# Performance work log

Measured on AMD Instinct MI355X. Metric: run time of the kernel, lower is better.

## Reference

```python
import jax, jax.numpy as jnp
import numpy as np

N_NEURONS, RANK, N_CONV, LY, LX, BATCH = 8192, 1, 64, 36, 36, 256


def setup_inputs() -> dict:
    key = jax.random.key(0)
    k1, k2, k3, k4 = jax.random.split(key, 4)
    conv = jax.random.normal(k1, (BATCH, N_CONV, LY, LX), dtype=jnp.float32)
    Wc = 0.01 * jax.random.normal(k2, (N_NEURONS, RANK, N_CONV), dtype=jnp.float32)
    Wy = 0.01 * jax.random.normal(k3, (N_NEURONS, RANK, LY), dtype=jnp.float32)
    Wx = 0.01 * jax.random.normal(k4, (N_NEURONS, RANK, LX), dtype=jnp.float32)
    bias = jnp.zeros((N_NEURONS,), dtype=jnp.float32)
    return {"conv": conv, "Wc": Wc, "Wy": Wy, "Wx": Wx, "bias": bias}


def reference(conv, Wc, Wy, Wx, bias):
    # yx_separable, rank == 1 path of Readout.forward:
    #   pred = einsum('nrc,nry,icyx,nrx->in', Wc, Wy, conv, Wx)
    #   pred = elu(pred + bias)
    # Staged contraction: build per-neuron rank-1 spatial filter, contract
    # spatial dims first (small y*x=1296), then channels.
    Wyx = jnp.einsum('nry,nrx->nryx', Wy, Wx)              # [N, R, Ly, Lx]
    s = jnp.einsum('icyx,nryx->inrc', conv, Wyx)           # [B, N, R, C]
    pred = jnp.einsum('inrc,nrc->in', s, Wc)               # [B, N]
    return jax.nn.elu(pred + bias)
```

## Files before the change

### kernel.cpp

```cpp
#include <hip/hip_runtime.h>
#include <hip/hip_bf16.h>

#define NNEUR 8192
#define NCONV 64
#define LYC   36
#define LXC   36
#define BATCH 256
#define KRAW  1296
#define KPAD  1344
#define KITER 21
#define MROWS 16384
#define BM 256
#define BN 128
#define BK 64
#define ACH_PER_IT 2048
#define BCH_PER_IT 1024
#define A_TILE_H   (KITER * ACH_PER_IT * 8)
#define B_TILE_H   (KITER * BCH_PER_IT * 8)

typedef __attribute__((ext_vector_type(8))) _Float16 half8;
typedef __attribute__((ext_vector_type(4))) float f32x4;
typedef __attribute__((ext_vector_type(16))) float f32x16;

__device__ __forceinline__ void async_copy16(const void* g, void* l) {
  __builtin_amdgcn_global_load_lds(
      (const __attribute__((address_space(1))) void*)g,
      (__attribute__((address_space(3))) void*)l, 16, 0, 0);
}

__global__ __launch_bounds__(256) void prep_kernel(
    const float* __restrict__ conv, const float* __restrict__ Wy,
    const float* __restrict__ Wx, _Float16* __restrict__ A,
    _Float16* __restrict__ B) {
  const int t = threadIdx.x;
  const int bx = blockIdx.x;
  const int tile = blockIdx.y;
  const int slot = t & 7;
  half8 h;
  if (bx < 168) {
    const int it = bx >> 3, i = bx & 7;
    const int r = (t >> 3) + 32 * i;
    const int c = (slot - r) & 7;
    const int k0 = it * 64 + c * 8;
    const int grow = tile * BM + r;
    if (k0 < KRAW) {
      const float* s = conv + (size_t)grow * KRAW + k0;
#pragma unroll
      for (int e = 0; e < 8; e++) h[e] = (_Float16)s[e];
    } else {
#pragma unroll
      for (int e = 0; e < 8; e++) h[e] = (_Float16)0.f;
    }
    *(half8*)(A + (size_t)tile * A_TILE_H + ((size_t)bx * 256 + t) * 8) = h;
  } else {
    const int bx4 = bx - 168;
    const int it = bx4 >> 2, i = bx4 & 3;
    const int r = (t >> 3) + 32 * i;
    const int c = (slot - r) & 7;
    const int k0 = it * 64 + c * 8;
    const int n = tile * BN + r;
#pragma unroll
    for (int e = 0; e < 8; e++) {
      const int k = k0 + e;
      float v = 0.f;
      if (k < KRAW) {
        const int y = k / LXC;
        const int x = k - y * LXC;
        v = Wy[n * LYC + y] * Wx[n * LXC + x] * 256.f;
      }
      h[e] = (_Float16)v;
    }
    *(half8*)(B + (size_t)tile * B_TILE_H + ((size_t)bx4 * 256 + t) * 8) = h;
  }
}

__global__ __launch_bounds__(256, 3) void gemm_fused_kernel(
    const _Float16* __restrict__ A, const _Float16* __restrict__ B,
    const float* __restrict__ Wc, const float* __restrict__ bias,
    float* __restrict__ out) {
  __shared__ _Float16 As[BM * BK];
  __shared__ _Float16 Bs[BN * BK];

  const int bid = blockIdx.x;
  const int l = bid >> 3;
  const int ntile = (bid & 7) * 8 + (l & 7);
  const int mtile = l >> 3;
  const int tileN = ntile * BN;
  const int tileM = mtile * BM;

  const int t = threadIdx.x;
  const int lane = t & 63;
  const int wave = t >> 6;
  const int wm = wave >> 1, wn = wave & 1;
  const int r32 = lane & 31, hh = lane >> 5;

  f32x16 acc[4][2] = {};

  const _Float16* pA = A + (size_t)mtile * A_TILE_H;
  const _Float16* pB = B + (size_t)ntile * B_TILE_H;
  _Float16* lA = As + t * 8;
  _Float16* lB = Bs + t * 8;

  for (int it = 0; it < KITER; it++) {
    const _Float16* sA = pA + (size_t)it * (ACH_PER_IT * 8) + t * 8;
    const _Float16* sB = pB + (size_t)it * (BCH_PER_IT * 8) + t * 8;
#pragma unroll
    for (int i = 0; i < 8; i++) async_copy16(sA + i * 2048, lA + i * 2048);
#pragma unroll
    for (int i = 0; i < 4; i++) async_copy16(sB + i * 2048, lB + i * 2048);
    __syncthreads();

#pragma unroll
    for (int ks = 0; ks < 4; ks++) {
      const int cc = 2 * ks + hh;
      half8 bf[2];
#pragma unroll
      for (int nb = 0; nb < 2; nb++) {
        const int r = wn * 64 + nb * 32 + r32;
        bf[nb] = *(const half8*)(Bs + r * 64 + ((cc + r) & 7) * 8);
      }
#pragma unroll
      for (int mb = 0; mb < 4; mb++) {
        const int r = wm * 128 + mb * 32 + r32;
        const half8 af = *(const half8*)(As + r * 64 + ((cc + r) & 7) * 8);
#pragma unroll
        for (int nb = 0; nb < 2; nb++)
          acc[mb][nb] = __builtin_amdgcn_mfma_f32_32x32x16_f16(
              af, bf[nb], acc[mb][nb], 0, 0, 0);
      }
    }
    __syncthreads();
  }

  const int ibase = mtile * 4 + wm * 2;
  float v[2][2];
#pragma unroll
  for (int nb = 0; nb < 2; nb++) {
    const int n_g = tileN + wn * 64 + nb * 32 + r32;
    const float* wc = Wc + (size_t)n_g * NCONV;
    f32x4 w[2][4];
#pragma unroll
    for (int hf = 0; hf < 2; hf++)
#pragma unroll
      for (int g = 0; g < 4; g++)
        w[hf][g] = *(const f32x4*)(wc + hf * 32 + hh * 4 + g * 8);
#pragma unroll
    for (int img = 0; img < 2; img++) {
      float p = 0.f;
#pragma unroll
      for (int hf = 0; hf < 2; hf++)
#pragma unroll
        for (int g = 0; g < 4; g++)
#pragma unroll
          for (int q = 0; q < 4; q++)
            p += acc[img * 2 + hf][nb][g * 4 + q] * w[hf][g][q];
      p += __shfl_xor(p, 32);
      v[img][nb] = p;
    }
  }
  const int img = ibase + hh;
#pragma unroll
  for (int nb = 0; nb < 2; nb++) {
    const int n_out = tileN + wn * 64 + nb * 32 + r32;
    float z = v[hh][nb] * 0.00390625f + bias[n_out];
    z = z > 0.f ? z : (__expf(z) - 1.f);
    out[(size_t)img * NNEUR + n_out] = z;
  }
}

extern "C" void kernel_launch(void* const* d_in, const int* in_sizes, int n_in,
                              void* d_out, int out_size, void* d_ws,
                              size_t ws_size, hipStream_t stream) {
  const float* conv = (const float*)d_in[0];
  const float* Wc = (const float*)d_in[1];
  const float* Wy = (const float*)d_in[2];
  const float* Wx = (const float*)d_in[3];
  const float* bias = (const float*)d_in[4];
  float* out = (float*)d_out;

  _Float16* Abuf = (_Float16*)d_ws;
  _Float16* Bbuf = (_Float16*)((char*)d_ws + (size_t)MROWS * KPAD * 2);

  prep_kernel<<<dim3(252, 64), 256, 0, stream>>>(conv, Wy, Wx, Abuf, Bbuf);
  gemm_fused_kernel<<<4096, 256, 0, stream>>>(Abuf, Bbuf, Wc, bias, out);
}
```

Measured before the change: 482.4 us.

## Double-buffer LDS tiles and enlarge GEMM block to 256x256 with 8 waves

Changes the GEMM tile from 256x128 to 256x256 with 512 threads (8 waves, 2x4 layout), which halves the grid and reuses each A tile across twice as many neurons. It adds double-buffered LDS so the async global-to-LDS copies for the next K step overlap with MFMA work on the current one, using manual vmcnt waits and barriers. It also raises wave priority around the MFMA loop. The prep kernel's B layout is reorganised to match the 256-wide N tiles. The costs are higher LDS use (128KB per block), possibly lower occupancy, and the risk of ordering errors in the hand-written waitcnt.

```diff
diff --git a/kernel.cpp b/kernel.cpp
--- a/kernel.cpp
+++ b/kernel.cpp
@@ -11,12 +11,11 @@
 #define KITER 21
 #define MROWS 16384
 #define BM 256
-#define BN 128
+#define BN 256
 #define BK 64
-#define ACH_PER_IT 2048
-#define BCH_PER_IT 1024
-#define A_TILE_H   (KITER * ACH_PER_IT * 8)
-#define B_TILE_H   (KITER * BCH_PER_IT * 8)
+#define A_IT_H   16384
+#define A_TILE_H (KITER * A_IT_H)
+#define B_TILE_H (KITER * A_IT_H)
 
 typedef __attribute__((ext_vector_type(8))) _Float16 half8;
 typedef __attribute__((ext_vector_type(4))) float f32x4;
@@ -34,10 +33,10 @@
     _Float16* __restrict__ B) {
   const int t = threadIdx.x;
   const int bx = blockIdx.x;
-  const int tile = blockIdx.y;
   const int slot = t & 7;
   half8 h;
   if (bx < 168) {
+    const int tile = blockIdx.y;
     const int it = bx >> 3, i = bx & 7;
     const int r = (t >> 3) + 32 * i;
     const int c = (slot - r) & 7;
@@ -53,12 +52,14 @@
     }
     *(half8*)(A + (size_t)tile * A_TILE_H + ((size_t)bx * 256 + t) * 8) = h;
   } else {
-    const int bx4 = bx - 168;
-    const int it = bx4 >> 2, i = bx4 & 3;
-    const int r = (t >> 3) + 32 * i;
+    const int bxp = bx - 168;
+    const int it = bxp >> 2, i4 = bxp & 3;
+    const int yb = blockIdx.y & 1;
+    const int ntile = blockIdx.y >> 1;
+    const int r = (t >> 3) + 32 * i4 + 128 * yb;
     const int c = (slot - r) & 7;
     const int k0 = it * 64 + c * 8;
-    const int n = tile * BN + r;
+    const int n = ntile * BN + r;
 #pragma unroll
     for (int e = 0; e < 8; e++) {
       const int k = k0 + e;
@@ -70,46 +71,47 @@
       }
       h[e] = (_Float16)v;
     }
-    *(half8*)(B + (size_t)tile * B_TILE_H + ((size_t)bx4 * 256 + t) * 8) = h;
-  }
-}
-
-__global__ __launch_bounds__(256, 3) void gemm_fused_kernel(
+    *(half8*)(B + (size_t)ntile * B_TILE_H + (size_t)it * A_IT_H +
+              (size_t)(yb * 1024 + i4 * 256 + t) * 8) = h;
+  }
+}
+
+__global__ __launch_bounds__(512, 2) void gemm_fused_kernel(
     const _Float16* __restrict__ A, const _Float16* __restrict__ B,
     const float* __restrict__ Wc, const float* __restrict__ bias,
     float* __restrict__ out) {
-  __shared__ _Float16 As[BM * BK];
-  __shared__ _Float16 Bs[BN * BK];
+  __shared__ _Float16 As[2][BM * BK];
+  __shared__ _Float16 Bs[2][BN * BK];
 
   const int bid = blockIdx.x;
-  const int l = bid >> 3;
-  const int ntile = (bid & 7) * 8 + (l & 7);
-  const int mtile = l >> 3;
+  const int gid = (bid & 7) * 256 + (bid >> 3);
+  const int mtile = gid >> 5;
+  const int ntile = gid & 31;
   const int tileN = ntile * BN;
-  const int tileM = mtile * BM;
 
   const int t = threadIdx.x;
   const int lane = t & 63;
   const int wave = t >> 6;
-  const int wm = wave >> 1, wn = wave & 1;
+  const int wm = wave >> 2, wn = wave & 3;
   const int r32 = lane & 31, hh = lane >> 5;
 
   f32x16 acc[4][2] = {};
 
-  const _Float16* pA = A + (size_t)mtile * A_TILE_H;
-  const _Float16* pB = B + (size_t)ntile * B_TILE_H;
-  _Float16* lA = As + t * 8;
-  _Float16* lB = Bs + t * 8;
-
-  for (int it = 0; it < KITER; it++) {
-    const _Float16* sA = pA + (size_t)it * (ACH_PER_IT * 8) + t * 8;
-    const _Float16* sB = pB + (size_t)it * (BCH_PER_IT * 8) + t * 8;
-#pragma unroll
-    for (int i = 0; i < 8; i++) async_copy16(sA + i * 2048, lA + i * 2048);
-#pragma unroll
-    for (int i = 0; i < 4; i++) async_copy16(sB + i * 2048, lB + i * 2048);
-    __syncthreads();
-
+  const _Float16* pA = A + (size_t)mtile * A_TILE_H + t * 8;
+  const _Float16* pB = B + (size_t)ntile * B_TILE_H + t * 8;
+
+  auto stage = [&](int b, int it) {
+    const _Float16* sA = pA + it * A_IT_H;
+    const _Float16* sB = pB + it * A_IT_H;
+    _Float16* lA = &As[b][t * 8];
+    _Float16* lB = &Bs[b][t * 8];
+#pragma unroll
+    for (int i = 0; i < 4; i++) async_copy16(sA + i * 4096, lA + i * 4096);
+#pragma unroll
+    for (int i = 0; i < 4; i++) async_copy16(sB + i * 4096, lB + i * 4096);
+  };
+
+  auto compute = [&](int b) {
 #pragma unroll
     for (int ks = 0; ks < 4; ks++) {
       const int cc = 2 * ks + hh;
@@ -117,20 +119,34 @@
 #pragma unroll
       for (int nb = 0; nb < 2; nb++) {
         const int r = wn * 64 + nb * 32 + r32;
-        bf[nb] = *(const half8*)(Bs + r * 64 + ((cc + r) & 7) * 8);
+        bf[nb] = *(const half8*)(&Bs[b][r * 64 + ((cc + r) & 7) * 8]);
       }
+      __builtin_amdgcn_s_setprio(1);
 #pragma unroll
       for (int mb = 0; mb < 4; mb++) {
         const int r = wm * 128 + mb * 32 + r32;
-        const half8 af = *(const half8*)(As + r * 64 + ((cc + r) & 7) * 8);
+        const half8 af = *(const half8*)(&As[b][r * 64 + ((cc + r) & 7) * 8]);
 #pragma unroll
         for (int nb = 0; nb < 2; nb++)
           acc[mb][nb] = __builtin_amdgcn_mfma_f32_32x32x16_f16(
               af, bf[nb], acc[mb][nb], 0, 0, 0);
       }
-    }
-    __syncthreads();
-  }
+      __builtin_amdgcn_s_setprio(0);
+    }
+  };
+
+  stage(0, 0);
+#pragma unroll 1
+  for (int it = 0; it < KITER - 1; ++it) {
+    stage((it + 1) & 1, it + 1);
+    asm volatile("s_waitcnt vmcnt(8)" ::: "memory");
+    __builtin_amdgcn_s_barrier();
+    compute(it & 1);
+    __builtin_amdgcn_s_barrier();
+  }
+  asm volatile("s_waitcnt vmcnt(0)" ::: "memory");
+  __builtin_amdgcn_s_barrier();
+  compute((KITER - 1) & 1);
 
   const int ibase = mtile * 4 + wm * 2;
   float v[2][2];
@@ -182,5 +198,5 @@
   _Float16* Bbuf = (_Float16*)((char*)d_ws + (size_t)MROWS * KPAD * 2);
 
   prep_kernel<<<dim3(252, 64), 256, 0, stream>>>(conv, Wy, Wx, Abuf, Bbuf);
-  gemm_fused_kernel<<<4096, 256, 0, stream>>>(Abuf, Bbuf, Wc, bias, out);
-}
+  gemm_fused_kernel<<<2048, 512, 0, stream>>>(Abuf, Bbuf, Wc, bias, out);
+}
```

New measurement: 503.2 us. 1.04x slower.
